# Performance work log

Measured on AMD Instinct MI355X. Metric: run time of the kernel, lower is better.

## Reference

```python
import jax, jax.numpy as jnp
import numpy as np

B, T, IN, H, N, W, R, NW, OUT = 16, 64, 256, 512, 256, 64, 4, 1, 256
NM = 1 + 2 * NW  # read modes
EPS = 1e-6

# interface slice offsets
_sizes = [R*W, R, NW*W, NW, NW*W, NW*W, R, NW, NW, R*NM]
_offs = np.concatenate([[0], np.cumsum(_sizes)])

def _oneplus(x):
    return 1.0 + jax.nn.softplus(x)

def _content_weights(M, keys, strengths):
    # M: [B,N,W], keys: [B,h,W], strengths: [B,h] -> [B,h,N]
    Mn = M / (jnp.linalg.norm(M, axis=-1, keepdims=True) + EPS)
    kn = keys / (jnp.linalg.norm(keys, axis=-1, keepdims=True) + EPS)
    sim = jnp.einsum('bnw,bhw->bhn', Mn, kn)
    return jax.nn.softmax(_oneplus(strengths)[..., None] * sim, axis=-1)

def setup_inputs() -> dict:
    key = jax.random.key(0)
    ks = jax.random.split(key, 5)
    s = 0.02
    return {
        'inputs': jax.random.normal(ks[0], (T, B, IN), jnp.float32),
        'W_ih': jax.random.normal(ks[1], (4*H, IN + R*W), jnp.float32) * s,
        'W_hh': jax.random.normal(ks[2], (4*H, H), jnp.float32) * s,
        'b_ih': jnp.zeros((4*H,), jnp.float32),
        'b_hh': jnp.zeros((4*H,), jnp.float32),
        'W_int': jax.random.normal(ks[3], (H, int(_offs[-1])), jnp.float32) * s,
        'b_int': jnp.zeros((int(_offs[-1]),), jnp.float32),
        'W_out': jax.random.normal(ks[4], (OUT, H + R*W), jnp.float32) * s,
        'b_out': jnp.zeros((OUT,), jnp.float32),
    }

def _dnc_forward(inputs, W_ih, W_hh, b_ih, b_hh, W_int, b_int, W_out, b_out):
    off_diag = 1.0 - jnp.eye(N, dtype=inputs.dtype)

    def step(carry, x_t):
        h, c, M, usage, link, prec, wr, ww_prev, read_words = carry
        ctrl_in = jnp.concatenate([x_t, read_words.reshape(B, -1)], axis=1)
        gates = ctrl_in @ W_ih.T + h @ W_hh.T + (b_ih + b_hh)
        i, f, g, o = jnp.split(gates, 4, axis=1)  # torch LSTM gate order
        c = jax.nn.sigmoid(f) * c + jax.nn.sigmoid(i) * jnp.tanh(g)
        h = jax.nn.sigmoid(o) * jnp.tanh(c)

        itf = h @ W_int + b_int
        def sl(j, shape):
            return itf[:, _offs[j]:_offs[j+1]].reshape((B,) + shape)
        read_keys = sl(0, (R, W)); read_str = sl(1, (R,))
        write_keys = sl(2, (NW, W)); write_str = sl(3, (NW,))
        erase = jax.nn.sigmoid(sl(4, (NW, W)))
        write_vec = jax.nn.sigmoid(sl(5, (NW, W)))
        free_gate = jax.nn.sigmoid(sl(6, (R,)))
        alloc_gate = jax.nn.sigmoid(sl(7, (NW,)))
        write_gate = jax.nn.sigmoid(sl(8, (NW,)))
        modes = jax.nn.softmax(sl(9, (R, NM)), axis=2)

        # usage with previous write weights and free gates over previous reads
        psi = jnp.prod(1.0 - free_gate[:, :, None] * wr, axis=1)  # [B,N]
        ww_agg = 1.0 - jnp.prod(1.0 - ww_prev, axis=1)
        usage = (usage + ww_agg - usage * ww_agg) * psi

        # allocation weighting (sort ascending usage)
        idx = jnp.argsort(usage, axis=1)
        u_s = jnp.take_along_axis(usage, idx, axis=1)
        prod_excl = jnp.cumprod(jnp.concatenate([jnp.ones((B, 1), usage.dtype), u_s[:, :-1]], axis=1), axis=1)
        a_s = (1.0 - u_s) * prod_excl
        alloc = jnp.zeros_like(usage).at[jnp.arange(B)[:, None], idx].set(a_s)

        cw = _content_weights(M, write_keys, write_str)  # [B,NW,N]
        ww = write_gate[..., None] * (alloc_gate[..., None] * alloc[:, None, :] + (1.0 - alloc_gate[..., None]) * cw)

        # memory erase + write
        M = M * jnp.prod(1.0 - ww[:, :, :, None] * erase[:, :, None, :], axis=1)
        M = M + jnp.einsum('bhn,bhw->bnw', ww, write_vec)

        # temporal link update (uses old precedence)
        ww_i = ww[..., :, None]; ww_j = ww[..., None, :]
        link = (1.0 - ww_i - ww_j) * link + ww_i * prec[:, :, None, :]
        link = link * off_diag
        prec = (1.0 - ww.sum(-1, keepdims=True)) * prec + ww

        fwd = jnp.einsum('bwij,brj->brwi', link, wr)
        bwd = jnp.einsum('bwji,brj->brwi', link, wr)
        cr = _content_weights(M, read_keys, read_str)  # [B,R,N]
        mb, mf, mc = modes[..., :NW], modes[..., NW:2*NW], modes[..., 2*NW]
        wr = jnp.einsum('brw,brwn->brn', mb, bwd) + jnp.einsum('brw,brwn->brn', mf, fwd) + mc[..., None] * cr
        read_words = jnp.einsum('brn,bnw->brw', wr, M)

        pre = jnp.concatenate([h, read_words.reshape(B, -1)], axis=1)
        out = pre @ W_out.T + b_out
        return (h, c, M, usage, link, prec, wr, ww, read_words), out

    z = jnp.zeros
    dt = inputs.dtype
    carry0 = (z((B, H), dt), z((B, H), dt), z((B, N, W), dt), z((B, N), dt),
              z((B, NW, N, N), dt), z((B, NW, N), dt), z((B, R, N), dt),
              z((B, NW, N), dt), z((B, R, W), dt))
    _, outs = jax.lax.scan(step, carry0, inputs)
    return outs  # [T,B,OUT]

def reference(inputs, W_ih, W_hh, b_ih, b_hh, W_int, b_int, W_out, b_out):
    return _dnc_forward(inputs, W_ih, W_hh, b_ih, b_hh, W_int, b_int, W_out, b_out)
```

## Files before the change

### kernel.cpp

```cpp
#include <hip/hip_runtime.h>
#include <math.h>

#define BT 256
#define GRID 144

#define Bx 16
#define Tt 64

__device__ __forceinline__ float sigm(float v) { return 1.0f / (1.0f + expf(-v)); }
__device__ __forceinline__ float oneplusf(float v) { return 1.0f + ((v > 15.0f) ? v : log1pf(expf(v))); }
__device__ __forceinline__ float4 ld4(const float* p) { return *reinterpret_cast<const float4*>(p); }
__device__ __forceinline__ float2 ld2f(const float* p) { return *reinterpret_cast<const float2*>(p); }

#define SCOPE_A __HIP_MEMORY_SCOPE_AGENT
__device__ __forceinline__ float gld(const float* p) {
    return __hip_atomic_load(p, __ATOMIC_RELAXED, SCOPE_A);
}
__device__ __forceinline__ void gst(float* p, float v) {
    __hip_atomic_store(p, v, __ATOMIC_RELAXED, SCOPE_A);
}
__device__ __forceinline__ float2 gld2(const float* p) {
    union { unsigned long long u; float2 f; } c;
    c.u = __hip_atomic_load(reinterpret_cast<const unsigned long long*>(p), __ATOMIC_RELAXED, SCOPE_A);
    return c.f;
}
__device__ __forceinline__ void gst2(float* p, float a, float b2) {
    union { unsigned long long u; float2 f; } c;
    c.f.x = a; c.f.y = b2;
    __hip_atomic_store(reinterpret_cast<unsigned long long*>(p), c.u, __ATOMIC_RELAXED, SCOPE_A);
}
__device__ __forceinline__ unsigned gldU(const unsigned* p) {
    return __hip_atomic_load(p, __ATOMIC_RELAXED, SCOPE_A);
}
__device__ __forceinline__ void gstU(unsigned* p, unsigned v) {
    __hip_atomic_store(p, v, __ATOMIC_RELAXED, SCOPE_A);
}

__device__ unsigned int g_flags[GRID];
__device__ unsigned int g_gen = 0;

__device__ __forceinline__ void gsync(unsigned tgt) {
    asm volatile("" ::: "memory");
    __builtin_amdgcn_s_waitcnt(0);
    __syncthreads();
    const int tid = threadIdx.x;
    if (blockIdx.x == 0) {
        if (tid < GRID) {
            if (tid == 0) gstU(&g_flags[0], tgt);
            while (gldU(&g_flags[tid]) < tgt) __builtin_amdgcn_s_sleep(1);
        }
        __syncthreads();
        if (tid == 0) gstU(&g_gen, tgt);
    } else {
        if (tid == 0) {
            gstU(&g_flags[blockIdx.x], tgt);
            while (gldU(&g_gen) < tgt) __builtin_amdgcn_s_sleep(1);
        }
        __syncthreads();
    }
    asm volatile("" ::: "memory");
}

#define ZERO_FLOATS 1376256

__global__ __launch_bounds__(BT)
void k_dnc(const float* __restrict__ x,
           const float* __restrict__ W_ih, const float* __restrict__ W_hh,
           const float* __restrict__ b_ih, const float* __restrict__ b_hh,
           const float* __restrict__ W_int, const float* __restrict__ b_int,
           const float* __restrict__ W_out, const float* __restrict__ b_out,
           float* __restrict__ outp, float* __restrict__ ws)
{
    const int bl = blockIdx.x, tid = threadIdx.x;

    float* h0   = ws;
    float* h1   = ws + 8192;
    float* cst  = ws + 16384;
    float* Mb   = ws + 24576;
    float* usg  = ws + 286720;
    float* lnk  = ws + 290816;
    float* pr0  = ws + 1339392;
    float* pr1  = ws + 1343488;
    float* wrb  = ws + 1347584;
    float* wwb  = ws + 1363968;
    float* rwb  = ws + 1368064;
    float* nrm  = ws + 1372160;
    float* itf  = ws + 1376256;
    float* ers  = ws + 1383792;
    float* wvs  = ws + 1384816;
    float* rso  = ws + 1385840;
    float* mds  = ws + 1385904;
    float* oh   = ws + 1386096;
    float* bwdb = ws + 1402480;
    float* fwdb = ws + 1418864;

    __shared__ __align__(16) float sbig[16576];
    __shared__ __align__(16) float smem[4096];
    __shared__ int s_idx[256];
    __shared__ unsigned s_base;

    if (tid == 0) s_base = gldU(&g_gen);
    __syncthreads();
    unsigned bseq = s_base;

    for (int i = bl * BT + tid; i < ZERO_FLOATS; i += GRID * BT) gst(ws + i, 0.0f);
    gsync(++bseq);

    for (int t = 0; t < Tt; ++t) {
        const float* hr = (t & 1) ? h1 : h0;
        float*       hw = (t & 1) ? h0 : h1;
        const float* pr_r = (t & 1) ? pr1 : pr0;
        float*       pr_w = (t & 1) ? pr0 : pr1;

        if (bl < 128) {
            {
                const float* xb = x + (size_t)t * (Bx * 256);
                for (int i = tid; i < 2048; i += BT) {
                    int b2 = i >> 7, q = (i & 127) * 2;
                    float2 v = ld2f(xb + b2 * 256 + q);
                    *reinterpret_cast<float2*>(&sbig[b2 * 260 + q]) = v;
                }
                for (int i = tid; i < 2048; i += BT) {
                    int b2 = i >> 7, q = (i & 127) * 2;
                    float2 v = gld2(rwb + b2 * 256 + q);
                    *reinterpret_cast<float2*>(&sbig[4160 + b2 * 260 + q]) = v;
                }
                for (int i = tid; i < 4096; i += BT) {
                    int b2 = i >> 8, q = (i & 255) * 2;
                    float2 v = gld2(hr + b2 * 512 + q);
                    *reinterpret_cast<float2*>(&sbig[8320 + b2 * 516 + q]) = v;
                }
            }
            __syncthreads();
            float* red = smem;
            int pl = tid >> 2, ks = tid & 3;
            int p = bl * 64 + pl;
            int b = p & 15, j = p >> 4;
            const float *w0, *w1, *w2, *w3;
            int kofs = (ks < 2) ? ks * 256 : (ks - 2) * 256;
            if (ks < 2) {
                w0 = W_ih + (j)        * 512 + kofs;
                w1 = W_ih + (j + 512)  * 512 + kofs;
                w2 = W_ih + (j + 1024) * 512 + kofs;
                w3 = W_ih + (j + 1536) * 512 + kofs;
            } else {
                w0 = W_hh + (j)        * 512 + kofs;
                w1 = W_hh + (j + 512)  * 512 + kofs;
                w2 = W_hh + (j + 1024) * 512 + kofs;
                w3 = W_hh + (j + 1536) * 512 + kofs;
            }
            const float* s = (ks == 0) ? &sbig[b * 260]
                           : (ks == 1) ? &sbig[4160 + b * 260]
                           :             &sbig[8320 + b * 516 + (ks - 2) * 256];
            float a0 = 0, a1 = 0, a2 = 0, a3 = 0;
            for (int kk = 0; kk < 256; kk += 4) {
                float4 iv = *reinterpret_cast<const float4*>(s + kk);
                float4 q0 = ld4(w0 + kk);
                a0 += iv.x * q0.x + iv.y * q0.y + iv.z * q0.z + iv.w * q0.w;
                float4 q1 = ld4(w1 + kk);
                a1 += iv.x * q1.x + iv.y * q1.y + iv.z * q1.z + iv.w * q1.w;
                float4 q2 = ld4(w2 + kk);
                a2 += iv.x * q2.x + iv.y * q2.y + iv.z * q2.z + iv.w * q2.w;
                float4 q3 = ld4(w3 + kk);
                a3 += iv.x * q3.x + iv.y * q3.y + iv.z * q3.z + iv.w * q3.w;
            }
            __syncthreads();
            red[pl * 16 + 0 * 4 + ks] = a0;
            red[pl * 16 + 1 * 4 + ks] = a1;
            red[pl * 16 + 2 * 4 + ks] = a2;
            red[pl * 16 + 3 * 4 + ks] = a3;
            __syncthreads();
            if (ks == 0) {
                const float* rp = red + pl * 16;
                float gi = rp[0]  + rp[1]  + rp[2]  + rp[3]  + b_ih[j]        + b_hh[j];
                float gf = rp[4]  + rp[5]  + rp[6]  + rp[7]  + b_ih[j + 512]  + b_hh[j + 512];
                float gg = rp[8]  + rp[9]  + rp[10] + rp[11] + b_ih[j + 1024] + b_hh[j + 1024];
                float go = rp[12] + rp[13] + rp[14] + rp[15] + b_ih[j + 1536] + b_hh[j + 1536];
                float cv = cst[b * 512 + j];
                cv = sigm(gf) * cv + sigm(gi) * tanhf(gg);
                float hv = sigm(go) * tanhf(cv);
                cst[b * 512 + j] = cv;
                gst(hw + b * 512 + j, hv);
            }
        } else if (t > 0) {
            int b = bl - 128;
            if (tid < 128) {
                float2 v = gld2(rwb + b * 256 + tid * 2);
                *reinterpret_cast<float2*>(&smem[tid * 2]) = v;
            }
            __syncthreads();
            int o = tid;
            float acc = b_out[o];
            acc += gld(oh + b * 256 + o) + gld(oh + (16 + b) * 256 + o)
                 + gld(oh + (32 + b) * 256 + o) + gld(oh + (48 + b) * 256 + o);
            const float* wrow = W_out + o * 768 + 512;
            for (int k = 0; k < 256; k += 4) {
                float4 w4 = ld4(wrow + k);
                float4 s4 = *reinterpret_cast<const float4*>(&smem[k]);
                acc += s4.x * w4.x + s4.y * w4.y + s4.z * w4.z + s4.w * w4.w;
            }
            outp[((size_t)(t - 1) * Bx + b) * 256 + o] = acc;
        }
        gsync(++bseq);

        if (bl < 15) {
            for (int i = tid; i < 4096; i += BT) {
                int b2 = i >> 8, q = (i & 255) * 2;
                float2 v = gld2(hw + b2 * 512 + q);
                *reinterpret_cast<float2*>(&sbig[b2 * 512 + q]) = v;
            }
            __syncthreads();
            int jl = tid & 31, k8 = tid >> 5;
            int j = bl * 32 + jl;
            float acc[16];
#pragma unroll
            for (int b = 0; b < 16; b++) acc[b] = 0.f;
            if (j < 471) {
                for (int k = k8 * 64; k < k8 * 64 + 64; ++k) {
                    float wv = W_int[k * 471 + j];
#pragma unroll
                    for (int b = 0; b < 16; b++) acc[b] += sbig[b * 512 + k] * wv;
                }
            }
            __syncthreads();
#pragma unroll
            for (int b = 0; b < 16; b++) smem[tid * 16 + b] = acc[b];
            __syncthreads();
            int jl2 = tid & 31, bh = tid >> 5;
            int j2 = bl * 32 + jl2;
            for (int rep = 0; rep < 2; ++rep) {
                int b2 = bh + 8 * rep;
                if (j2 < 471) {
                    float s = 0;
#pragma unroll
                    for (int ksx = 0; ksx < 8; ksx++) s += smem[(ksx * 32 + jl2) * 16 + b2];
                    gst(itf + b2 * 471 + j2, s + b_int[j2]);
                }
            }
        } else if (bl < 79) {
            int idx = bl - 15;
            int b = idx >> 2, ks = idx & 3;
            if (tid < 64) {
                float2 v = gld2(hw + b * 512 + ks * 128 + tid * 2);
                *reinterpret_cast<float2*>(&smem[tid * 2]) = v;
            }
            __syncthreads();
            int o = tid;
            const float* wrow = W_out + o * 768 + ks * 128;
            float acc = 0;
            for (int k = 0; k < 128; k += 4) {
                float4 w4 = ld4(wrow + k);
                float4 s4 = *reinterpret_cast<const float4*>(&smem[k]);
                acc += s4.x * w4.x + s4.y * w4.y + s4.z * w4.z + s4.w * w4.w;
            }
            gst(oh + (ks * 16 + b) * 256 + o, acc);
        }
        gsync(++bseq);

        if (bl < 16) {
            const int b = bl;
            for (int i = tid; i < 8192; i += BT) {
                int n = i >> 5, w2 = (i & 31) * 2;
                float2 v = gld2(Mb + (b * 256 + n) * 64 + w2);
                sbig[w2 * 256 + ((n + w2) & 255)] = v.x;
                sbig[(w2 + 1) * 256 + ((n + w2 + 1) & 255)] = v.y;
            }
            float* s_keys = smem;
            float* s_cw   = smem + 256;
            float* s_al   = smem + 512;
            float* s_tmp  = smem + 768;
            float* s_wk   = smem + 1024;
            float* s_sc   = smem + 1088;
            const float* it = itf + b * 471;

            gst(bwdb + b * 1024 + tid, 0.f);
            gst(bwdb + b * 1024 + 256 + tid, 0.f);
            gst(bwdb + b * 1024 + 512 + tid, 0.f);
            gst(bwdb + b * 1024 + 768 + tid, 0.f);

            if (tid < 4) {
                float m0 = gld(it + 459 + tid * 3), m1 = gld(it + 460 + tid * 3), m2 = gld(it + 461 + tid * 3);
                float mx3 = fmaxf(m0, fmaxf(m1, m2));
                float e0 = expf(m0 - mx3), e1 = expf(m1 - mx3), e2 = expf(m2 - mx3);
                float inv = 1.f / (e0 + e1 + e2);
                gst(mds + (b * 4 + tid) * 3 + 0, e0 * inv);
                gst(mds + (b * 4 + tid) * 3 + 1, e1 * inv);
                gst(mds + (b * 4 + tid) * 3 + 2, e2 * inv);
                gst(rso + b * 4 + tid, oneplusf(gld(it + 256 + tid)));
                s_sc[tid] = sigm(gld(it + 453 + tid));
            }
            if (tid == 4) s_sc[4] = sigm(gld(it + 457));
            if (tid == 5) s_sc[5] = sigm(gld(it + 458));
            if (tid == 6) s_sc[6] = oneplusf(gld(it + 324));
            if (tid < 64) {
                gst(ers + b * 64 + tid, sigm(gld(it + 325 + tid)));
                gst(wvs + b * 64 + tid, sigm(gld(it + 389 + tid)));
                s_wk[tid] = gld(it + 260 + tid);
            }
            __syncthreads();
            if (tid < 64) {
                float v = s_wk[tid] * s_wk[tid];
                for (int o2 = 32; o2 > 0; o2 >>= 1) v += __shfl_down(v, o2);
                if (tid == 0) s_sc[7] = sqrtf(v);
            }
            __syncthreads();
            {
                int n = tid;
                float psi = 1.f;
#pragma unroll
                for (int r = 0; r < 4; r++) psi *= (1.f - s_sc[r] * gld(wrb + b * 1024 + r * 256 + n));
                float wwp = gld(wwb + b * 256 + n);
                float u = usg[b * 256 + n];
                u = (u + wwp - u * wwp) * psi;
                usg[b * 256 + n] = u;
                s_keys[n] = u; s_idx[n] = n;
                float dot = 0.f;
                for (int w = 0; w < 64; ++w)
                    dot += sbig[w * 256 + ((n + w) & 255)] * s_wk[w];
                s_cw[n] = s_sc[6] * dot / ((gld(nrm + b * 256 + n) + 1e-6f) * (s_sc[7] + 1e-6f));
            }
            __syncthreads();
            s_tmp[tid] = s_cw[tid];
            __syncthreads();
            for (int s2 = 128; s2 > 0; s2 >>= 1) { if (tid < s2) s_tmp[tid] = fmaxf(s_tmp[tid], s_tmp[tid + s2]); __syncthreads(); }
            float mx = s_tmp[0];
            __syncthreads();
            float ex = expf(s_cw[tid] - mx);
            s_tmp[tid] = ex;
            __syncthreads();
            for (int s2 = 128; s2 > 0; s2 >>= 1) { if (tid < s2) s_tmp[tid] += s_tmp[tid + s2]; __syncthreads(); }
            float cwv = ex / s_tmp[0];
            __syncthreads();
            s_cw[tid] = cwv;
            for (int kk2 = 2; kk2 <= 256; kk2 <<= 1) {
                for (int j2 = kk2 >> 1; j2 > 0; j2 >>= 1) {
                    int ixj = tid ^ j2;
                    if (ixj > tid) {
                        float ka = s_keys[tid], kb = s_keys[ixj];
                        int ia = s_idx[tid], ib = s_idx[ixj];
                        bool up = ((tid & kk2) == 0);
                        bool sw = up ? (kb < ka || (kb == ka && ib < ia))
                                     : (ka < kb || (ka == kb && ia < ib));
                        if (sw) { s_keys[tid] = kb; s_keys[ixj] = ka; s_idx[tid] = ib; s_idx[ixj] = ia; }
                    }
                    __syncthreads();
                }
            }
            s_tmp[tid] = s_keys[tid];
            __syncthreads();
            for (int o2 = 1; o2 < 256; o2 <<= 1) {
                float pv = (tid >= o2) ? s_tmp[tid - o2] : 1.0f;
                __syncthreads();
                s_tmp[tid] *= pv;
                __syncthreads();
            }
            float excl = (tid == 0) ? 1.0f : s_tmp[tid - 1];
            float a_s = (1.0f - s_keys[tid]) * excl;
            s_al[s_idx[tid]] = a_s;
            __syncthreads();
            float ag = s_sc[4], wg = s_sc[5];
            float wwn = wg * (ag * s_al[tid] + (1.f - ag) * s_cw[tid]);
            gst(wwb + b * 256 + tid, wwn);
            s_tmp[tid] = wwn;
            __syncthreads();
            for (int s2 = 128; s2 > 0; s2 >>= 1) { if (tid < s2) s_tmp[tid] += s_tmp[tid + s2]; __syncthreads(); }
            float S = s_tmp[0];
            gst(pr_w + b * 256 + tid, (1.f - S) * gld(pr_r + b * 256 + tid) + wwn);
        }
        gsync(++bseq);

        if (bl < 128) {
            int b = bl >> 3, ch = bl & 7;
            int ci = tid;
            float* s_wrL = smem;
            float* s_ww  = smem + 1024;
            float* s_fp  = smem + 1280;
            {
                float2 v0 = gld2(wrb + b * 1024 + tid * 4);
                float2 v1 = gld2(wrb + b * 1024 + tid * 4 + 2);
                s_wrL[tid * 4 + 0] = v0.x; s_wrL[tid * 4 + 1] = v0.y;
                s_wrL[tid * 4 + 2] = v1.x; s_wrL[tid * 4 + 3] = v1.y;
                s_ww[tid] = gld(wwb + b * 256 + tid);
            }
            __syncthreads();
            float wwc = s_ww[ci];
            float pco = gld(pr_r + b * 256 + ci);
            float* Lb = lnk + b * 65536;
            float b0 = 0, b1 = 0, b2 = 0, b3 = 0;
            int r0 = ch * 32;
            int wv = tid >> 6, lane = tid & 63;
            for (int rr = 0; rr < 32; ++rr) {
                int ri = r0 + rr;
                float wwr = s_ww[ri];
                float v = Lb[ri * 256 + ci];
                v = (1.f - wwr - wwc) * v + wwr * pco;
                if (ci == ri) v = 0.f;
                Lb[ri * 256 + ci] = v;
                b0 += v * s_wrL[ri];
                b1 += v * s_wrL[256 + ri];
                b2 += v * s_wrL[512 + ri];
                b3 += v * s_wrL[768 + ri];
                float p0 = v * s_wrL[ci];
                float p1 = v * s_wrL[256 + ci];
                float p2 = v * s_wrL[512 + ci];
                float p3 = v * s_wrL[768 + ci];
                for (int o2 = 32; o2 > 0; o2 >>= 1) {
                    p0 += __shfl_down(p0, o2); p1 += __shfl_down(p1, o2);
                    p2 += __shfl_down(p2, o2); p3 += __shfl_down(p3, o2);
                }
                if (lane == 0) {
                    s_fp[(rr * 4 + 0) * 4 + wv] = p0;
                    s_fp[(rr * 4 + 1) * 4 + wv] = p1;
                    s_fp[(rr * 4 + 2) * 4 + wv] = p2;
                    s_fp[(rr * 4 + 3) * 4 + wv] = p3;
                }
            }
            __syncthreads();
            if (tid < 128) {
                int rr = tid >> 2, r = tid & 3;
                const float* fp = s_fp + (rr * 4 + r) * 4;
                gst(fwdb + b * 1024 + r * 256 + (r0 + rr), fp[0] + fp[1] + fp[2] + fp[3]);
            }
            atomicAdd(bwdb + b * 1024 + ci, b0);
            atomicAdd(bwdb + b * 1024 + 256 + ci, b1);
            atomicAdd(bwdb + b * 1024 + 512 + ci, b2);
            atomicAdd(bwdb + b * 1024 + 768 + ci, b3);
        } else {
            int b = bl - 128;
            if (tid < 32) {
                float2 v = gld2(ers + b * 64 + tid * 2);
                *reinterpret_cast<float2*>(&smem[tid * 2]) = v;
            } else if (tid < 64) {
                int q = tid - 32;
                float2 v = gld2(wvs + b * 64 + q * 2);
                *reinterpret_cast<float2*>(&smem[64 + q * 2]) = v;
            } else if (tid < 192) {
                int q = tid - 64;
                float2 v = gld2(wwb + b * 256 + q * 2);
                *reinterpret_cast<float2*>(&smem[128 + q * 2]) = v;
            }
            __syncthreads();
            int w2g = (tid & 31) * 2, ng = tid >> 5;
            for (int i = 0; i < 32; ++i) {
                int n = ng * 32 + i;
                float wwn = smem[128 + n];
                float2 m = gld2(Mb + (b * 256 + n) * 64 + w2g);
                m.x = m.x * (1.f - wwn * smem[w2g])     + wwn * smem[64 + w2g];
                m.y = m.y * (1.f - wwn * smem[w2g + 1]) + wwn * smem[64 + w2g + 1];
                gst2(Mb + (b * 256 + n) * 64 + w2g, m.x, m.y);
                float s = m.x * m.x + m.y * m.y;
                for (int o2 = 16; o2 > 0; o2 >>= 1) s += __shfl_down(s, o2, 32);
                if (w2g == 0) gst(nrm + b * 256 + n, sqrtf(s));
            }
        }
        gsync(++bseq);

        if (bl < 64) {
            int b = bl >> 2, r = bl & 3;
            for (int i = tid; i < 8192; i += BT) {
                int n = i >> 5, w2 = (i & 31) * 2;
                float2 v = gld2(Mb + (b * 256 + n) * 64 + w2);
                sbig[w2 * 256 + ((n + w2) & 255)] = v.x;
                sbig[(w2 + 1) * 256 + ((n + w2 + 1) & 255)] = v.y;
            }
            float* s_wr  = smem;
            float* s_tmp = smem + 512;
            float* s_key = smem + 768;
            float* s_sc  = smem + 840;
            s_wr[tid] = gld(wrb + b * 1024 + r * 256 + tid);
            if (tid < 64) s_key[tid] = gld(itf + b * 471 + r * 64 + tid);
            __syncthreads();
            if (tid < 64) {
                float v = s_key[tid] * s_key[tid];
                for (int o2 = 32; o2 > 0; o2 >>= 1) v += __shfl_down(v, o2);
                if (tid == 0) s_sc[0] = sqrtf(v);
            }
            __syncthreads();
            int n = tid;
            float bwd_n = gld(bwdb + b * 1024 + r * 256 + n);
            float fwd_n = gld(fwdb + b * 1024 + r * 256 + n);
            float dot = 0.f;
            for (int w = 0; w < 64; ++w)
                dot += sbig[w * 256 + ((n + w) & 255)] * s_key[w];
            float simv = gld(rso + b * 4 + r) * dot / ((gld(nrm + b * 256 + n) + 1e-6f) * (s_sc[0] + 1e-6f));
            s_tmp[tid] = simv;
            __syncthreads();
            for (int s2 = 128; s2 > 0; s2 >>= 1) { if (tid < s2) s_tmp[tid] = fmaxf(s_tmp[tid], s_tmp[tid + s2]); __syncthreads(); }
            float mx = s_tmp[0];
            __syncthreads();
            float ex = expf(simv - mx);
            s_tmp[tid] = ex;
            __syncthreads();
            for (int s2 = 128; s2 > 0; s2 >>= 1) { if (tid < s2) s_tmp[tid] += s_tmp[tid + s2]; __syncthreads(); }
            float crv = ex / s_tmp[0];
            float mbv = gld(mds + (b * 4 + r) * 3 + 0);
            float mfv = gld(mds + (b * 4 + r) * 3 + 1);
            float mcv = gld(mds + (b * 4 + r) * 3 + 2);
            float wrn = mbv * bwd_n + mfv * fwd_n + mcv * crv;
            gst(wrb + b * 1024 + r * 256 + n, wrn);
            __syncthreads();
            s_wr[tid] = wrn;
            __syncthreads();
            int w = tid & 63, gq = tid >> 6;
            float pacc = 0.f;
            for (int k = 0; k < 64; ++k) {
                int n2 = gq * 64 + k;
                pacc += s_wr[n2] * sbig[w * 256 + ((n2 + w) & 255)];
            }
            s_tmp[tid] = pacc;
            __syncthreads();
            if (tid < 64)
                gst(rwb + b * 256 + r * 64 + tid,
                    s_tmp[tid] + s_tmp[tid + 64] + s_tmp[tid + 128] + s_tmp[tid + 192]);
        }
        gsync(++bseq);
    }

    if (bl < 16) {
        int b = bl;
        if (tid < 128) {
            float2 v = gld2(rwb + b * 256 + tid * 2);
            *reinterpret_cast<float2*>(&smem[tid * 2]) = v;
        }
        __syncthreads();
        int o = tid;
        float acc = b_out[o];
        acc += gld(oh + b * 256 + o) + gld(oh + (16 + b) * 256 + o)
             + gld(oh + (32 + b) * 256 + o) + gld(oh + (48 + b) * 256 + o);
        const float* wrow = W_out + o * 768 + 512;
        for (int k = 0; k < 256; k += 4) {
            float4 w4 = ld4(wrow + k);
            float4 s4 = *reinterpret_cast<const float4*>(&smem[k]);
            acc += s4.x * w4.x + s4.y * w4.y + s4.z * w4.z + s4.w * w4.w;
        }
        outp[((size_t)(Tt - 1) * Bx + b) * 256 + o] = acc;
    }
}

extern "C" void kernel_launch(void* const* d_in, const int* in_sizes, int n_in,
                              void* d_out, int out_size, void* d_ws, size_t ws_size,
                              hipStream_t stream) {
    const float* x     = (const float*)d_in[0];
    const float* W_ih  = (const float*)d_in[1];
    const float* W_hh  = (const float*)d_in[2];
    const float* b_ih  = (const float*)d_in[3];
    const float* b_hh  = (const float*)d_in[4];
    const float* W_int = (const float*)d_in[5];
    const float* b_int = (const float*)d_in[6];
    const float* W_out = (const float*)d_in[7];
    const float* b_out = (const float*)d_in[8];
    float* outp = (float*)d_out;
    float* ws   = (float*)d_ws;
    (void)in_sizes; (void)n_in; (void)out_size; (void)ws_size;

    k_dnc<<<GRID, BT, 0, stream>>>(x, W_ih, W_hh, b_ih, b_hh, W_int, b_int,
                                   W_out, b_out, outp, ws);
}
```

Before: 9.051 ms.

## Fuse interface projection into write-head phase and replace bitonic sort with rank sort

The interface-vector matmul (h @ W_int) moves into the per-batch write-head blocks, so each of 16 blocks computes its own 471-wide itf row locally. This removes one grid-wide barrier per timestep. The W_out partial products run concurrently in blocks 16-79. The bitonic sort with its many __syncthreads is replaced by an O(N) per-thread rank computation plus a wave-shuffle cumulative product. The trade-off is that each write block now does the full 512x471 matvec alone, which is more serial work per block, and the global sync flags are given 128-byte alignment.

```diff
diff --git a/kernel.cpp b/kernel.cpp
--- a/kernel.cpp
+++ b/kernel.cpp
@@ -36,8 +36,8 @@
     __hip_atomic_store(p, v, __ATOMIC_RELAXED, SCOPE_A);
 }
 
-__device__ unsigned int g_flags[GRID];
-__device__ unsigned int g_gen = 0;
+__device__ __attribute__((aligned(128))) unsigned int g_flags[GRID];
+__device__ __attribute__((aligned(128))) unsigned int g_gen = 0;
 
 __device__ __forceinline__ void gsync(unsigned tgt) {
     asm volatile("" ::: "memory");
@@ -203,99 +203,78 @@
         }
         gsync(++bseq);
 
-        if (bl < 15) {
-            for (int i = tid; i < 4096; i += BT) {
-                int b2 = i >> 8, q = (i & 255) * 2;
-                float2 v = gld2(hw + b2 * 512 + q);
-                *reinterpret_cast<float2*>(&sbig[b2 * 512 + q]) = v;
-            }
-            __syncthreads();
-            int jl = tid & 31, k8 = tid >> 5;
-            int j = bl * 32 + jl;
-            float acc[16];
-#pragma unroll
-            for (int b = 0; b < 16; b++) acc[b] = 0.f;
-            if (j < 471) {
-                for (int k = k8 * 64; k < k8 * 64 + 64; ++k) {
-                    float wv = W_int[k * 471 + j];
-#pragma unroll
-                    for (int b = 0; b < 16; b++) acc[b] += sbig[b * 512 + k] * wv;
-                }
-            }
-            __syncthreads();
-#pragma unroll
-            for (int b = 0; b < 16; b++) smem[tid * 16 + b] = acc[b];
-            __syncthreads();
-            int jl2 = tid & 31, bh = tid >> 5;
-            int j2 = bl * 32 + jl2;
-            for (int rep = 0; rep < 2; ++rep) {
-                int b2 = bh + 8 * rep;
-                if (j2 < 471) {
-                    float s = 0;
-#pragma unroll
-                    for (int ksx = 0; ksx < 8; ksx++) s += smem[(ksx * 32 + jl2) * 16 + b2];
-                    gst(itf + b2 * 471 + j2, s + b_int[j2]);
-                }
-            }
-        } else if (bl < 79) {
-            int idx = bl - 15;
-            int b = idx >> 2, ks = idx & 3;
-            if (tid < 64) {
-                float2 v = gld2(hw + b * 512 + ks * 128 + tid * 2);
-                *reinterpret_cast<float2*>(&smem[tid * 2]) = v;
-            }
-            __syncthreads();
-            int o = tid;
-            const float* wrow = W_out + o * 768 + ks * 128;
-            float acc = 0;
-            for (int k = 0; k < 128; k += 4) {
-                float4 w4 = ld4(wrow + k);
-                float4 s4 = *reinterpret_cast<const float4*>(&smem[k]);
-                acc += s4.x * w4.x + s4.y * w4.y + s4.z * w4.z + s4.w * w4.w;
-            }
-            gst(oh + (ks * 16 + b) * 256 + o, acc);
-        }
-        gsync(++bseq);
-
         if (bl < 16) {
             const int b = bl;
-            for (int i = tid; i < 8192; i += BT) {
-                int n = i >> 5, w2 = (i & 31) * 2;
-                float2 v = gld2(Mb + (b * 256 + n) * 64 + w2);
-                sbig[w2 * 256 + ((n + w2) & 255)] = v.x;
-                sbig[(w2 + 1) * 256 + ((n + w2 + 1) & 255)] = v.y;
-            }
             float* s_keys = smem;
             float* s_cw   = smem + 256;
             float* s_al   = smem + 512;
             float* s_tmp  = smem + 768;
             float* s_wk   = smem + 1024;
             float* s_sc   = smem + 1088;
-            const float* it = itf + b * 471;
-
+            float* s_h    = smem + 1152;
+            float* s_itf  = smem + 1664;
+            float* s_part = smem + 2176;
+
+            for (int i = tid; i < 8192; i += BT) {
+                int n = i >> 5, w2 = (i & 31) * 2;
+                float2 v = gld2(Mb + (b * 256 + n) * 64 + w2);
+                sbig[w2 * 256 + ((n + w2) & 255)] = v.x;
+                sbig[(w2 + 1) * 256 + ((n + w2 + 1) & 255)] = v.y;
+            }
+            {
+                float2 v = gld2(hw + b * 512 + tid * 2);
+                *reinterpret_cast<float2*>(&s_h[tid * 2]) = v;
+            }
             gst(bwdb + b * 1024 + tid, 0.f);
             gst(bwdb + b * 1024 + 256 + tid, 0.f);
             gst(bwdb + b * 1024 + 512 + tid, 0.f);
             gst(bwdb + b * 1024 + 768 + tid, 0.f);
-
+            __syncthreads();
+
+            {
+                int jp = tid & 127, kh = tid >> 7;
+                for (int r2 = 0; r2 < 2; ++r2) {
+                    int j0 = (r2 * 128 + jp) * 2;
+                    float a0 = 0.f, a1 = 0.f;
+                    if (j0 < 471) {
+                        const float* wc = W_int + j0;
+                        for (int k = kh * 256; k < kh * 256 + 256; ++k) {
+                            float2 wv = ld2f(wc + k * 471);
+                            float hv = s_h[k];
+                            a0 += hv * wv.x;
+                            a1 += hv * wv.y;
+                        }
+                    }
+                    s_part[kh * 512 + jp * 2]     = a0;
+                    s_part[kh * 512 + jp * 2 + 1] = a1;
+                    __syncthreads();
+                    int j = r2 * 256 + tid;
+                    if (j < 471)
+                        s_itf[j] = s_part[tid] + s_part[512 + tid] + b_int[j];
+                    __syncthreads();
+                }
+            }
+            gst(itf + b * 471 + tid, s_itf[tid]);
+
+            const float* it = s_itf;
             if (tid < 4) {
-                float m0 = gld(it + 459 + tid * 3), m1 = gld(it + 460 + tid * 3), m2 = gld(it + 461 + tid * 3);
+                float m0 = it[459 + tid * 3], m1 = it[460 + tid * 3], m2 = it[461 + tid * 3];
                 float mx3 = fmaxf(m0, fmaxf(m1, m2));
                 float e0 = expf(m0 - mx3), e1 = expf(m1 - mx3), e2 = expf(m2 - mx3);
                 float inv = 1.f / (e0 + e1 + e2);
                 gst(mds + (b * 4 + tid) * 3 + 0, e0 * inv);
                 gst(mds + (b * 4 + tid) * 3 + 1, e1 * inv);
                 gst(mds + (b * 4 + tid) * 3 + 2, e2 * inv);
-                gst(rso + b * 4 + tid, oneplusf(gld(it + 256 + tid)));
-                s_sc[tid] = sigm(gld(it + 453 + tid));
-            }
-            if (tid == 4) s_sc[4] = sigm(gld(it + 457));
-            if (tid == 5) s_sc[5] = sigm(gld(it + 458));
-            if (tid == 6) s_sc[6] = oneplusf(gld(it + 324));
+                gst(rso + b * 4 + tid, oneplusf(it[256 + tid]));
+                s_sc[tid] = sigm(it[453 + tid]);
+            }
+            if (tid == 4) s_sc[4] = sigm(it[457]);
+            if (tid == 5) s_sc[5] = sigm(it[458]);
+            if (tid == 6) s_sc[6] = oneplusf(it[324]);
             if (tid < 64) {
-                gst(ers + b * 64 + tid, sigm(gld(it + 325 + tid)));
-                gst(wvs + b * 64 + tid, sigm(gld(it + 389 + tid)));
-                s_wk[tid] = gld(it + 260 + tid);
+                gst(ers + b * 64 + tid, sigm(it[325 + tid]));
+                gst(wvs + b * 64 + tid, sigm(it[389 + tid]));
+                s_wk[tid] = it[260 + tid];
             }
             __syncthreads();
             if (tid < 64) {
@@ -313,7 +292,7 @@
                 float u = usg[b * 256 + n];
                 u = (u + wwp - u * wwp) * psi;
                 usg[b * 256 + n] = u;
-                s_keys[n] = u; s_idx[n] = n;
+                s_keys[n] = u;
                 float dot = 0.f;
                 for (int w = 0; w < 64; ++w)
                     dot += sbig[w * 256 + ((n + w) & 255)] * s_wk[w];
@@ -332,31 +311,35 @@
             float cwv = ex / s_tmp[0];
             __syncthreads();
             s_cw[tid] = cwv;
-            for (int kk2 = 2; kk2 <= 256; kk2 <<= 1) {
-                for (int j2 = kk2 >> 1; j2 > 0; j2 >>= 1) {
-                    int ixj = tid ^ j2;
-                    if (ixj > tid) {
-                        float ka = s_keys[tid], kb = s_keys[ixj];
-                        int ia = s_idx[tid], ib = s_idx[ixj];
-                        bool up = ((tid & kk2) == 0);
-                        bool sw = up ? (kb < ka || (kb == ka && ib < ia))
-                                     : (ka < kb || (ka == kb && ia < ib));
-                        if (sw) { s_keys[tid] = kb; s_keys[ixj] = ka; s_idx[tid] = ib; s_idx[ixj] = ia; }
-                    }
-                    __syncthreads();
-                }
-            }
-            s_tmp[tid] = s_keys[tid];
-            __syncthreads();
-            for (int o2 = 1; o2 < 256; o2 <<= 1) {
-                float pv = (tid >= o2) ? s_tmp[tid - o2] : 1.0f;
+
+            {
+                float myk = s_keys[tid];
                 __syncthreads();
-                s_tmp[tid] *= pv;
+                int rank = 0;
+                for (int j2 = 0; j2 < 256; ++j2) {
+                    float kj = s_keys[j2];
+                    rank += (kj < myk || (kj == myk && j2 < tid)) ? 1 : 0;
+                }
+                s_tmp[rank] = myk;
+                s_idx[rank] = tid;
                 __syncthreads();
-            }
-            float excl = (tid == 0) ? 1.0f : s_tmp[tid - 1];
-            float a_s = (1.0f - s_keys[tid]) * excl;
-            s_al[s_idx[tid]] = a_s;
+                int lane = tid & 63, wv = tid >> 6;
+                float v = s_tmp[tid];
+                float incl = v;
+                for (int off = 1; off < 64; off <<= 1) {
+                    float pp = __shfl_up(incl, off);
+                    if (lane >= off) incl *= pp;
+                }
+                if (lane == 63) s_wk[wv] = incl;
+                __syncthreads();
+                float wpre = 1.f;
+#pragma unroll
+                for (int q = 0; q < 4; ++q) if (q < wv) wpre *= s_wk[q];
+                float exin = __shfl_up(incl, 1);
+                float excl = wpre * ((lane == 0) ? 1.f : exin);
+                float a_s = (1.f - v) * excl;
+                s_al[s_idx[tid]] = a_s;
+            }
             __syncthreads();
             float ag = s_sc[4], wg = s_sc[5];
             float wwn = wg * (ag * s_al[tid] + (1.f - ag) * s_cw[tid]);
@@ -366,6 +349,23 @@
             for (int s2 = 128; s2 > 0; s2 >>= 1) { if (tid < s2) s_tmp[tid] += s_tmp[tid + s2]; __syncthreads(); }
             float S = s_tmp[0];
             gst(pr_w + b * 256 + tid, (1.f - S) * gld(pr_r + b * 256 + tid) + wwn);
+        } else if (bl < 80) {
+            int idx = bl - 16;
+            int b = idx >> 2, ks = idx & 3;
+            if (tid < 64) {
+                float2 v = gld2(hw + b * 512 + ks * 128 + tid * 2);
+                *reinterpret_cast<float2*>(&smem[tid * 2]) = v;
+            }
+            __syncthreads();
+            int o = tid;
+            const float* wrow = W_out + o * 768 + ks * 128;
+            float acc = 0;
+            for (int k = 0; k < 128; k += 4) {
+                float4 w4 = ld4(wrow + k);
+                float4 s4 = *reinterpret_cast<const float4*>(&smem[k]);
+                acc += s4.x * w4.x + s4.y * w4.y + s4.z * w4.z + s4.w * w4.w;
+            }
+            gst(oh + (ks * 16 + b) * 256 + o, acc);
         }
         gsync(++bseq);
 
```

After: 12.89 ms. +42.4%, slower.
